# Performance work log

Hardware: AMD Instinct MI355X
Metric: run time of the kernel (lower is better)

## Reference

```python
import jax, jax.numpy as jnp
import numpy as np

CHUNK = 64   # hyperparams['chunk_size']
HEADS = 16   # hyperparams['n_heads']


def _chunk_mask(T, cs):
    # Faithful reproduction of the original (buggy) chunked mask:
    # for chunk pair with q-chunk start i and k-chunk start j, masking is applied
    # only when i >= j, with triu(diagonal = j - i + 1). Algebraically this masks
    # position (q, k) iff q_block_start >= k_block_start and
    #   (k - q) - 2*(k_block_start - q_block_start) >= 1.
    idx = jnp.arange(T)
    blk = (idx // cs) * cs  # chunk start of each position
    qb = blk[:, None]
    kb = blk[None, :]
    masked = (qb >= kb) & ((idx[None, :] - idx[:, None] - 2 * (kb - qb)) >= 1)
    return masked  # [T, T], True = set score to -inf


def setup_inputs() -> dict:
    key = jax.random.key(0)
    ks = jax.random.split(key, 6)
    B, T, C = 2, 2048, 1024
    w = 0.02  # init scale so softmax is not saturated
    return {
        "x": jax.random.normal(ks[0], (B, T, C), jnp.float32),
        "Wq": jax.random.normal(ks[1], (C, C), jnp.float32) * w,
        "bq": jnp.zeros((C,), jnp.float32),
        "Wk": jax.random.normal(ks[2], (C, C), jnp.float32) * w,
        "bk": jnp.zeros((C,), jnp.float32),
        "Wv": jax.random.normal(ks[3], (C, C), jnp.float32) * w,
        "bv": jnp.zeros((C,), jnp.float32),
        "Wo": jax.random.normal(ks[4], (C, C), jnp.float32) * w,
        "bo": jnp.zeros((C,), jnp.float32),
        "attn_scale": jnp.full((1,), 1.0 / np.sqrt(C // HEADS), jnp.float32),
    }


def reference(x, Wq, bq, Wk, bk, Wv, bv, Wo, bo, attn_scale):
    B, T, C = x.shape
    H = HEADS
    D = C // H
    # torch nn.Linear: y = x @ W.T + b
    q = (x @ Wq.T + bq).reshape(B, T, H, D)
    k = (x @ Wk.T + bk).reshape(B, T, H, D)
    v = (x @ Wv.T + bv).reshape(B, T, H, D)
    scores = jnp.einsum("bqhd,bkhd->bhqk", q, k) * attn_scale[0]
    mask = _chunk_mask(T, CHUNK)  # [T, T]
    scores = jnp.where(mask[None, None], -jnp.inf, scores)
    attn = jax.nn.softmax(scores, axis=-1)  # [B, H, T, T]
    out = jnp.einsum("bhqk,bkhd->bqhd", attn, v).reshape(B, T, C)
    return out @ Wo.T + bo
```

## Files before the change

### kernel.cpp

```cpp
#include <hip/hip_runtime.h>


typedef __attribute__((ext_vector_type(8))) short bf16x8;
typedef __attribute__((ext_vector_type(4))) float f32x4;
typedef __attribute__((ext_vector_type(4))) float float4v;
typedef __attribute__((ext_vector_type(4))) unsigned short u16x4;

__device__ __forceinline__ unsigned short f2bf(float x){
  union { float f; unsigned int u; } c; c.f = x;
  unsigned int r = c.u + 0x7FFFu + ((c.u >> 16) & 1u);
  return (unsigned short)(r >> 16);
}
__device__ __forceinline__ float bf2f(unsigned short h){
  union { unsigned int u; float f; } c; c.u = ((unsigned int)h) << 16;
  return c.f;
}
__device__ __forceinline__ f32x4 zero4(){ f32x4 v; v[0]=0.f; v[1]=0.f; v[2]=0.f; v[3]=0.f; return v; }
__device__ __forceinline__ unsigned int cvtpk(float a, float b){
  unsigned int r;
  asm("v_cvt_pk_bf16_f32 %0, %1, %2" : "=v"(r) : "v"(a), "v"(b));
  return r;
}
__device__ __forceinline__ float exp2x(float x){
  float r;
  asm("v_exp_f32 %0, %1" : "=v"(r) : "v"(x));
  return r;
}

#define GLDS16(g, l) __builtin_amdgcn_global_load_lds( \
  (const __attribute__((address_space(1))) void*)(g), \
  (__attribute__((address_space(3))) void*)(l), 16, 0, 0)

__global__ __launch_bounds__(256) void k_prep(
    const float* __restrict__ x,
    const float* __restrict__ Wq, const float* __restrict__ Wk,
    const float* __restrict__ Wv, const float* __restrict__ Wo,
    const float* __restrict__ bq, const float* __restrict__ bk, const float* __restrict__ bv,
    unsigned short* __restrict__ xh, unsigned short* __restrict__ wh,
    float* __restrict__ bias_cat){
  const int NX = 1048576;
  const int NTOT = 2097152;
  int i = blockIdx.x * 256 + threadIdx.x;
  if (i < 3072){
    const float* bs[3] = {bq, bk, bv};
    bias_cat[i] = bs[i >> 10][i & 1023];
  }
  int stride = gridDim.x * 256;
  for (; i < NTOT; i += stride){
    float4v v;
    u16x4 h;
    if (i < NX){
      v = ((const float4v*)x)[i];
      #pragma unroll
      for (int j = 0; j < 4; ++j) h[j] = f2bf(v[j]);
      ((u16x4*)xh)[i] = h;
    } else {
      int jj = i - NX;
      const float* srcs[4] = {Wq, Wk, Wv, Wo};
      v = ((const float4v*)srcs[jj >> 18])[jj & 0x3FFFF];
      #pragma unroll
      for (int j = 0; j < 4; ++j) h[j] = f2bf(v[j]);
      ((u16x4*)wh)[jj] = h;
    }
  }
}

template<int BM, int BN, int MODE, int SPLITA>
__global__ __launch_bounds__(256) void k_gemm(
    const unsigned short* __restrict__ Ah, const unsigned short* __restrict__ Al,
    const unsigned short* __restrict__ Bh,
    const float* __restrict__ bias, const float* __restrict__ scale_p,
    unsigned short* __restrict__ oq, unsigned short* __restrict__ okk,
    unsigned short* __restrict__ ov, float* __restrict__ fo)
{
  constexpr int MF = (BN == 128) ? (BM/32) : (BM/64);
  constexpr int NF = 4;
  constexpr int AISS = BM/64;
  constexpr int BISS = BN/64;
  constexpr int NA = SPLITA ? 2 : 1;
  __shared__ unsigned short As[NA][BM*32];
  __shared__ unsigned short Bs[BN*32];

  const int tid  = threadIdx.x;
  const int wid  = tid >> 6;
  const int lane = tid & 63;
  const int l15  = lane & 15;
  const int kg   = lane >> 4;
  const int m0 = blockIdx.y * BM;
  const int n0 = blockIdx.x * BN;
  const int wrb = (BN == 128) ? (wid >> 1) * (BM/2) : wid * (BM/4);
  const int wcb = (BN == 128) ? (wid & 1) * 64 : 0;
  const float qs = (MODE == 0) ? scale_p[0] * 1.4426950408889634f : 0.f;

  f32x4 acc[MF][NF];
  #pragma unroll
  for (int a = 0; a < MF; ++a)
    #pragma unroll
    for (int b = 0; b < NF; ++b) acc[a][b] = zero4();

  for (int k0 = 0; k0 < 1024; k0 += 32){
    #pragma unroll
    for (int p = 0; p < NA; ++p){
      const unsigned short* Asrc = p ? Al : Ah;
      #pragma unroll
      for (int iss = 0; iss < AISS; ++iss){
        int L = iss*2048 + tid*8;
        int row = L >> 5;
        int ck = ((L >> 3) & 3) ^ ((row >> 1) & 3);
        GLDS16(Asrc + (size_t)(m0 + row)*1024 + k0 + ck*8,
               (char*)(&As[p][0]) + iss*4096 + wid*1024);
      }
    }
    #pragma unroll
    for (int iss = 0; iss < BISS; ++iss){
      int L = iss*2048 + tid*8;
      int row = L >> 5;
      int ck = ((L >> 3) & 3) ^ ((row >> 1) & 3);
      GLDS16(Bh + (size_t)(n0 + row)*1024 + k0 + ck*8,
             (char*)(&Bs[0]) + iss*4096 + wid*1024);
    }
    __syncthreads();

    bf16x8 af[MF][NA];
    #pragma unroll
    for (int mf = 0; mf < MF; ++mf){
      int r = wrb + mf*16 + l15;
      int ckpos = kg ^ ((r >> 1) & 3);
      #pragma unroll
      for (int p = 0; p < NA; ++p)
        af[mf][p] = *(const bf16x8*)((const char*)(&As[p][0]) + r*64 + ckpos*16);
    }
    #pragma unroll
    for (int nf = 0; nf < NF; ++nf){
      int r = wcb + nf*16 + l15;
      int ckpos = kg ^ ((r >> 1) & 3);
      bf16x8 bhv = *(const bf16x8*)((const char*)(&Bs[0]) + r*64 + ckpos*16);
      #pragma unroll
      for (int mf = 0; mf < MF; ++mf){
        acc[mf][nf] = __builtin_amdgcn_mfma_f32_16x16x32_bf16(af[mf][0], bhv, acc[mf][nf], 0,0,0);
        if (SPLITA)
          acc[mf][nf] = __builtin_amdgcn_mfma_f32_16x16x32_bf16(af[mf][1], bhv, acc[mf][nf], 0,0,0);
      }
    }
    __syncthreads();
  }

  #pragma unroll
  for (int mf = 0; mf < MF; ++mf){
    #pragma unroll
    for (int nf = 0; nf < NF; ++nf){
      int colg = n0 + wcb + nf*16 + l15;
      float bb = bias[colg];
      #pragma unroll
      for (int j = 0; j < 4; ++j){
        int r = m0 + wrb + mf*16 + kg*4 + j;
        float val = acc[mf][nf][j] + bb;
        if (MODE == 1){
          fo[(size_t)r*1024 + colg] = val;
        } else {
          int bi = r >> 11, tt = r & 2047;
          int mat = colg >> 10, jj = colg & 1023;
          int h = jj >> 6, d = jj & 63;
          size_t bh_ = (size_t)(bi*16 + h);
          if (mat == 0)      oq [(bh_*2048 + tt)*64 + d] = f2bf(val * qs);
          else if (mat == 1) okk[(bh_*2048 + tt)*64 + d] = f2bf(val);
          else               ov [(bh_*64 + d)*2048 + tt] = f2bf(val);
        }
      }
    }
  }
}

__global__ __launch_bounds__(256) void k_attn(
    const unsigned short* __restrict__ Qg, const unsigned short* __restrict__ Kg,
    const unsigned short* __restrict__ Vtg,
    unsigned short* __restrict__ Ohi, unsigned short* __restrict__ Olo)
{
  __shared__ unsigned short Qs[64*64];
  __shared__ unsigned short Ks[2][64*64];
  __shared__ unsigned short Vts[2][64*64];

  const int tid  = threadIdx.x;
  const int wid  = tid >> 6;
  const int lane = tid & 63;
  const int l15  = lane & 15;
  const int kg   = lane >> 4;
  const int qi = blockIdx.x >> 5;
  const int bh = blockIdx.x & 31;
  const size_t base = (size_t)bh * (2048*64);

  const int r0 = tid >> 3;
  const int ck = ((tid & 7) ^ (r0 & 7)) * 8;
  const unsigned short* qp = Qg  + base + (size_t)(qi*64 + r0)*64 + ck;
  const unsigned short* kp = Kg  + base + (size_t)(qi*64 + r0)*64 + ck;
  const unsigned short* vp = Vtg + base + (size_t)r0*2048 + qi*64 + ck;

  GLDS16(qp,         (char*)Qs  + wid*1024);
  GLDS16(qp + 2048,  (char*)Qs  + wid*1024 + 4096);
  GLDS16(kp,         (char*)Ks  + wid*1024);
  GLDS16(kp + 2048,  (char*)Ks  + wid*1024 + 4096);
  GLDS16(vp,         (char*)Vts + wid*1024);
  GLDS16(vp + 65536, (char*)Vts + wid*1024 + 4096);
  kp += 4096;  vp += 64;
  __syncthreads();

  const int c0 = (kg ^ (l15 & 7)) << 4;
  const int c1 = c0 ^ 64;
  const char* qbase = (const char*)Qs + wid*2048 + l15*128;
  char* pwb = (char*)Qs + wid*2048 + l15*128;
  const int pws = (kg*8) ^ ((l15 & 7) << 4);

  const bf16x8 qf0 = *(const bf16x8*)(qbase + c0);
  const bf16x8 qf1 = *(const bf16x8*)(qbase + c1);

  f32x4 Ot[4];
  #pragma unroll
  for (int d = 0; d < 4; ++d) Ot[d] = zero4();
  float m = -1e30f, l = 0.f;
  const int qloc = wid*16 + l15;

  for (int kb = qi; kb < 32; ++kb){
    const int buf = (kb - qi) & 1;
    const char* ksb = (const char*)Ks  + buf*8192 + l15*128;
    const char* vsb = (const char*)Vts + buf*8192 + l15*128;
    if (kb + 1 < 32){
      char* dK = (char*)Ks  + (buf^1)*8192 + wid*1024;
      char* dV = (char*)Vts + (buf^1)*8192 + wid*1024;
      GLDS16(kp,         dK);
      GLDS16(kp + 2048,  dK + 4096);
      GLDS16(vp,         dV);
      GLDS16(vp + 65536, dV + 4096);
      kp += 4096;  vp += 64;
    }
    f32x4 ST[4];
    #pragma unroll
    for (int nf = 0; nf < 4; ++nf) ST[nf] = zero4();
    __builtin_amdgcn_s_setprio(1);
    #pragma unroll
    for (int nf = 0; nf < 4; ++nf){
      bf16x8 ak = *(const bf16x8*)(ksb + nf*2048 + c0);
      ST[nf] = __builtin_amdgcn_mfma_f32_16x16x32_bf16(ak, qf0, ST[nf], 0,0,0);
    }
    #pragma unroll
    for (int nf = 0; nf < 4; ++nf){
      bf16x8 ak = *(const bf16x8*)(ksb + nf*2048 + c1);
      ST[nf] = __builtin_amdgcn_mfma_f32_16x16x32_bf16(ak, qf1, ST[nf], 0,0,0);
    }
    __builtin_amdgcn_s_setprio(0);
    if (kb == qi){
      #pragma unroll
      for (int nf = 0; nf < 4; ++nf)
        #pragma unroll
        for (int j = 0; j < 4; ++j)
          if (nf*16 + kg*4 + j > qloc) ST[nf][j] = -1e30f;
    }
    float mx0 = fmaxf(fmaxf(ST[0][0], ST[0][1]), fmaxf(ST[0][2], ST[0][3]));
    float mx1 = fmaxf(fmaxf(ST[1][0], ST[1][1]), fmaxf(ST[1][2], ST[1][3]));
    float mx2 = fmaxf(fmaxf(ST[2][0], ST[2][1]), fmaxf(ST[2][2], ST[2][3]));
    float mx3 = fmaxf(fmaxf(ST[3][0], ST[3][1]), fmaxf(ST[3][2], ST[3][3]));
    float pmax = fmaxf(fmaxf(mx0, mx1), fmaxf(mx2, mx3));
    pmax = fmaxf(pmax, __shfl_xor(pmax, 16, 64));
    pmax = fmaxf(pmax, __shfl_xor(pmax, 32, 64));
    if (!__all(pmax <= m + 8.0f)){
      float mn = fmaxf(m, pmax);
      float fj = exp2x(m - mn);
      m = mn;
      l *= fj;
      #pragma unroll
      for (int df = 0; df < 4; ++df)
        #pragma unroll
        for (int j = 0; j < 4; ++j) Ot[df][j] *= fj;
    }
    float rsn[4];
    unsigned int pk[4][2];
    #pragma unroll
    for (int nf = 0; nf < 4; ++nf){
      float p0 = exp2x(ST[nf][0] - m), p1 = exp2x(ST[nf][1] - m);
      float p2 = exp2x(ST[nf][2] - m), p3 = exp2x(ST[nf][3] - m);
      rsn[nf] = (p0 + p1) + (p2 + p3);
      pk[nf][0] = cvtpk(p0, p1);
      pk[nf][1] = cvtpk(p2, p3);
    }
    float rs = (rsn[0] + rsn[1]) + (rsn[2] + rsn[3]);
    rs += __shfl_xor(rs, 16, 64);
    rs += __shfl_xor(rs, 32, 64);
    l += rs;
    #pragma unroll
    for (int nf = 0; nf < 4; ++nf)
      *(uint2*)(pwb + (pws ^ (nf*32))) = make_uint2(pk[nf][0], pk[nf][1]);
    {
      bf16x8 pa0 = *(const bf16x8*)(qbase + c0);
      bf16x8 pa1 = *(const bf16x8*)(qbase + c1);
      __builtin_amdgcn_s_setprio(1);
      #pragma unroll
      for (int df = 0; df < 4; ++df){
        bf16x8 vb = *(const bf16x8*)(vsb + df*2048 + c0);
        Ot[df] = __builtin_amdgcn_mfma_f32_16x16x32_bf16(vb, pa0, Ot[df], 0,0,0);
      }
      #pragma unroll
      for (int df = 0; df < 4; ++df){
        bf16x8 vb = *(const bf16x8*)(vsb + df*2048 + c1);
        Ot[df] = __builtin_amdgcn_mfma_f32_16x16x32_bf16(vb, pa1, Ot[df], 0,0,0);
      }
      __builtin_amdgcn_s_setprio(0);
    }
    __syncthreads();
  }

  const int bi = bh >> 4, h = bh & 15;
  const float rinv = 1.0f / l;
  const size_t row = (size_t)(bi*2048 + qi*64 + qloc);
  #pragma unroll
  for (int df = 0; df < 4; ++df){
    int colb = h*64 + df*16 + kg*4;
    u16x4 hv, lv;
    #pragma unroll
    for (int j = 0; j < 4; ++j){
      float v = Ot[df][j] * rinv;
      unsigned short hvv = f2bf(v);
      hv[j] = hvv;
      lv[j] = f2bf(v - bf2f(hvv));
    }
    *(u16x4*)(Ohi + row*1024 + colb) = hv;
    *(u16x4*)(Olo + row*1024 + colb) = lv;
  }
}

extern "C" void kernel_launch(void* const* d_in, const int* in_sizes, int n_in,
                              void* d_out, int out_size, void* d_ws, size_t ws_size,
                              hipStream_t stream){
  const float* x  = (const float*)d_in[0];
  const float* Wq = (const float*)d_in[1];
  const float* bq = (const float*)d_in[2];
  const float* Wk = (const float*)d_in[3];
  const float* bk = (const float*)d_in[4];
  const float* Wv = (const float*)d_in[5];
  const float* bv = (const float*)d_in[6];
  const float* Wo = (const float*)d_in[7];
  const float* bo = (const float*)d_in[8];
  const float* scale = (const float*)d_in[9];
  float* out = (float*)d_out;

  char* ws = (char*)d_ws;
  const size_t MB = 1024*1024;
  unsigned short* xh  = (unsigned short*)(ws + 0*MB);
  unsigned short* wh  = (unsigned short*)(ws + 16*MB);
  unsigned short* Qb  = (unsigned short*)(ws + 32*MB);
  unsigned short* Kb  = (unsigned short*)(ws + 40*MB);
  unsigned short* Vtb = (unsigned short*)(ws + 48*MB);
  unsigned short* Ohi = (unsigned short*)(ws + 56*MB);
  unsigned short* Olo = (unsigned short*)(ws + 64*MB);
  float* bias_cat     = (float*)(ws + 72*MB);

  hipLaunchKernelGGL(k_prep, dim3(2048), dim3(256), 0, stream,
                     x, Wq, Wk, Wv, Wo, bq, bk, bv, xh, wh, bias_cat);
  hipLaunchKernelGGL((k_gemm<128,128,0,0>), dim3(24,32), dim3(256), 0, stream,
                     xh, (const unsigned short*)nullptr, wh, bias_cat, scale,
                     Qb, Kb, Vtb, (float*)nullptr);
  hipLaunchKernelGGL(k_attn, dim3(1024), dim3(256), 0, stream, Qb, Kb, Vtb, Ohi, Olo);
  hipLaunchKernelGGL((k_gemm<64,64,1,1>), dim3(16,64), dim3(256), 0, stream,
                     Ohi, Olo, wh + 3u*1048576u, bo, (const float*)nullptr,
                     (unsigned short*)nullptr, (unsigned short*)nullptr,
                     (unsigned short*)nullptr, out);
}
```

Measured before the change: 205.9 us.

## Pair attention tiles per block and software-pipeline QK with triple-buffered K/V

Each attention block now handles two query tiles, pr and 31-pr, so the causal (upper-triangle) work is balanced across blocks, and the grid is halved. Inside the loop, QK^T for the next key tile is issued before the softmax and PV of the current tile. K and V use triple-buffered LDS with explicit vmcnt waits instead of __syncthreads, so loads and MFMA work overlap better. The cost is more LDS, more live registers (STn), and half as many blocks, which may leave some CUs idle.

```diff
diff --git a/kernel.cpp b/kernel.cpp
--- a/kernel.cpp
+++ b/kernel.cpp
@@ -25,6 +25,13 @@
   float r;
   asm("v_exp_f32 %0, %1" : "=v"(r) : "v"(x));
   return r;
+}
+__device__ __forceinline__ void wait_barrier(int n){
+  if (n == 4)      asm volatile("s_waitcnt vmcnt(4)" ::: "memory");
+  else if (n == 2) asm volatile("s_waitcnt vmcnt(2)" ::: "memory");
+  else             asm volatile("s_waitcnt vmcnt(0)" ::: "memory");
+  __builtin_amdgcn_s_barrier();
+  __builtin_amdgcn_sched_barrier(0);
 }
 
 #define GLDS16(g, l) __builtin_amdgcn_global_load_lds( \
@@ -176,153 +183,204 @@
     const unsigned short* __restrict__ Vtg,
     unsigned short* __restrict__ Ohi, unsigned short* __restrict__ Olo)
 {
-  __shared__ unsigned short Qs[64*64];
-  __shared__ unsigned short Ks[2][64*64];
-  __shared__ unsigned short Vts[2][64*64];
+  __shared__ unsigned short Qs[4096];
+  __shared__ unsigned short Ks[3][4096];
+  __shared__ unsigned short Vts[3][4096];
 
   const int tid  = threadIdx.x;
   const int wid  = tid >> 6;
   const int lane = tid & 63;
   const int l15  = lane & 15;
   const int kg   = lane >> 4;
-  const int qi = blockIdx.x >> 5;
+  const int pr = blockIdx.x >> 5;
   const int bh = blockIdx.x & 31;
   const size_t base = (size_t)bh * (2048*64);
 
   const int r0 = tid >> 3;
   const int ck = ((tid & 7) ^ (r0 & 7)) * 8;
-  const unsigned short* qp = Qg  + base + (size_t)(qi*64 + r0)*64 + ck;
-  const unsigned short* kp = Kg  + base + (size_t)(qi*64 + r0)*64 + ck;
-  const unsigned short* vp = Vtg + base + (size_t)r0*2048 + qi*64 + ck;
-
-  GLDS16(qp,         (char*)Qs  + wid*1024);
-  GLDS16(qp + 2048,  (char*)Qs  + wid*1024 + 4096);
-  GLDS16(kp,         (char*)Ks  + wid*1024);
-  GLDS16(kp + 2048,  (char*)Ks  + wid*1024 + 4096);
-  GLDS16(vp,         (char*)Vts + wid*1024);
-  GLDS16(vp + 65536, (char*)Vts + wid*1024 + 4096);
-  kp += 4096;  vp += 64;
-  __syncthreads();
-
   const int c0 = (kg ^ (l15 & 7)) << 4;
   const int c1 = c0 ^ 64;
   const char* qbase = (const char*)Qs + wid*2048 + l15*128;
   char* pwb = (char*)Qs + wid*2048 + l15*128;
   const int pws = (kg*8) ^ ((l15 & 7) << 4);
-
-  const bf16x8 qf0 = *(const bf16x8*)(qbase + c0);
-  const bf16x8 qf1 = *(const bf16x8*)(qbase + c1);
-
-  f32x4 Ot[4];
-  #pragma unroll
-  for (int d = 0; d < 4; ++d) Ot[d] = zero4();
-  float m = -1e30f, l = 0.f;
   const int qloc = wid*16 + l15;
-
-  for (int kb = qi; kb < 32; ++kb){
-    const int buf = (kb - qi) & 1;
-    const char* ksb = (const char*)Ks  + buf*8192 + l15*128;
-    const char* vsb = (const char*)Vts + buf*8192 + l15*128;
-    if (kb + 1 < 32){
-      char* dK = (char*)Ks  + (buf^1)*8192 + wid*1024;
-      char* dV = (char*)Vts + (buf^1)*8192 + wid*1024;
-      GLDS16(kp,         dK);
-      GLDS16(kp + 2048,  dK + 4096);
-      GLDS16(vp,         dV);
-      GLDS16(vp + 65536, dV + 4096);
-      kp += 4096;  vp += 64;
-    }
+  const int bi = bh >> 4, h = bh & 15;
+
+  #pragma unroll 1
+  for (int half = 0; half < 2; ++half){
+    const int t0 = half ? (31 - pr) : pr;
+    const unsigned short* qp  = Qg  + base + (size_t)(t0*64 + r0)*64 + ck;
+    const unsigned short* kp0 = Kg  + base + (size_t)(t0*64 + r0)*64 + ck;
+    const unsigned short* vp0 = Vtg + base + (size_t)r0*2048 + t0*64 + ck;
+    GLDS16(qp,          (char*)Qs + wid*1024);
+    GLDS16(qp + 2048,   (char*)Qs + wid*1024 + 4096);
+    GLDS16(kp0,         (char*)(&Ks[0][0]) + wid*1024);
+    GLDS16(kp0 + 2048,  (char*)(&Ks[0][0]) + wid*1024 + 4096);
+    GLDS16(vp0,         (char*)(&Vts[0][0]) + wid*1024);
+    GLDS16(vp0 + 65536, (char*)(&Vts[0][0]) + wid*1024 + 4096);
+    int nA = 0;
+    if (t0 + 1 <= 31){
+      GLDS16(kp0 + 4096, (char*)(&Ks[1][0]) + wid*1024);
+      GLDS16(kp0 + 6144, (char*)(&Ks[1][0]) + wid*1024 + 4096);
+      nA = 2;
+    }
+    wait_barrier(nA);
+
+    const bf16x8 qf0 = *(const bf16x8*)(qbase + c0);
+    const bf16x8 qf1 = *(const bf16x8*)(qbase + c1);
+
     f32x4 ST[4];
     #pragma unroll
     for (int nf = 0; nf < 4; ++nf) ST[nf] = zero4();
-    __builtin_amdgcn_s_setprio(1);
-    #pragma unroll
-    for (int nf = 0; nf < 4; ++nf){
-      bf16x8 ak = *(const bf16x8*)(ksb + nf*2048 + c0);
-      ST[nf] = __builtin_amdgcn_mfma_f32_16x16x32_bf16(ak, qf0, ST[nf], 0,0,0);
-    }
-    #pragma unroll
-    for (int nf = 0; nf < 4; ++nf){
-      bf16x8 ak = *(const bf16x8*)(ksb + nf*2048 + c1);
-      ST[nf] = __builtin_amdgcn_mfma_f32_16x16x32_bf16(ak, qf1, ST[nf], 0,0,0);
-    }
-    __builtin_amdgcn_s_setprio(0);
-    if (kb == qi){
+    {
+      const char* ksb = (const char*)(&Ks[0][0]) + l15*128;
+      __builtin_amdgcn_s_setprio(1);
+      #pragma unroll
+      for (int nf = 0; nf < 4; ++nf){
+        bf16x8 ak = *(const bf16x8*)(ksb + nf*2048 + c0);
+        ST[nf] = __builtin_amdgcn_mfma_f32_16x16x32_bf16(ak, qf0, ST[nf], 0,0,0);
+      }
+      #pragma unroll
+      for (int nf = 0; nf < 4; ++nf){
+        bf16x8 ak = *(const bf16x8*)(ksb + nf*2048 + c1);
+        ST[nf] = __builtin_amdgcn_mfma_f32_16x16x32_bf16(ak, qf1, ST[nf], 0,0,0);
+      }
+      __builtin_amdgcn_s_setprio(0);
+    }
+    #pragma unroll
+    for (int nf = 0; nf < 4; ++nf)
+      #pragma unroll
+      for (int j = 0; j < 4; ++j)
+        if (nf*16 + kg*4 + j > qloc) ST[nf][j] = -1e30f;
+
+    int nB = 0;
+    if (t0 + 1 <= 31){
+      GLDS16(vp0 + 64,         (char*)(&Vts[1][0]) + wid*1024);
+      GLDS16(vp0 + 64 + 65536, (char*)(&Vts[1][0]) + wid*1024 + 4096);
+      nB += 2;
+    }
+    if (t0 + 2 <= 31){
+      GLDS16(kp0 + 8192,  (char*)(&Ks[2][0]) + wid*1024);
+      GLDS16(kp0 + 10240, (char*)(&Ks[2][0]) + wid*1024 + 4096);
+      nB += 2;
+    }
+    wait_barrier(nB);
+
+    f32x4 Ot[4];
+    #pragma unroll
+    for (int d = 0; d < 4; ++d) Ot[d] = zero4();
+    float m = -1e30f, l = 0.f;
+    const unsigned short* kp = kp0 + 12288;
+    const unsigned short* vp = vp0 + 128;
+    int s0 = 0, s1 = 1, s2 = 2;
+
+    for (int kb = t0; kb < 32; ++kb){
+      int nIss = 0;
+      if (kb + 3 <= 31){
+        char* dK = (char*)(&Ks[s0][0]) + wid*1024;
+        GLDS16(kp, dK);
+        GLDS16(kp + 2048, dK + 4096);
+        kp += 4096; nIss += 2;
+      }
+      if (kb + 2 <= 31){
+        char* dV = (char*)(&Vts[s2][0]) + wid*1024;
+        GLDS16(vp, dV);
+        GLDS16(vp + 65536, dV + 4096);
+        vp += 64; nIss += 2;
+      }
+      f32x4 STn[4];
+      if (kb < 31){
+        const char* ksb = (const char*)(&Ks[s1][0]) + l15*128;
+        #pragma unroll
+        for (int nf = 0; nf < 4; ++nf) STn[nf] = zero4();
+        __builtin_amdgcn_s_setprio(1);
+        #pragma unroll
+        for (int nf = 0; nf < 4; ++nf){
+          bf16x8 ak = *(const bf16x8*)(ksb + nf*2048 + c0);
+          STn[nf] = __builtin_amdgcn_mfma_f32_16x16x32_bf16(ak, qf0, STn[nf], 0,0,0);
+        }
+        #pragma unroll
+        for (int nf = 0; nf < 4; ++nf){
+          bf16x8 ak = *(const bf16x8*)(ksb + nf*2048 + c1);
+          STn[nf] = __builtin_amdgcn_mfma_f32_16x16x32_bf16(ak, qf1, STn[nf], 0,0,0);
+        }
+        __builtin_amdgcn_s_setprio(0);
+      }
+      float mx0 = fmaxf(fmaxf(ST[0][0], ST[0][1]), fmaxf(ST[0][2], ST[0][3]));
+      float mx1 = fmaxf(fmaxf(ST[1][0], ST[1][1]), fmaxf(ST[1][2], ST[1][3]));
+      float mx2 = fmaxf(fmaxf(ST[2][0], ST[2][1]), fmaxf(ST[2][2], ST[2][3]));
+      float mx3 = fmaxf(fmaxf(ST[3][0], ST[3][1]), fmaxf(ST[3][2], ST[3][3]));
+      float pmax = fmaxf(fmaxf(mx0, mx1), fmaxf(mx2, mx3));
+      pmax = fmaxf(pmax, __shfl_xor(pmax, 16, 64));
+      pmax = fmaxf(pmax, __shfl_xor(pmax, 32, 64));
+      if (!__all(pmax <= m + 8.0f)){
+        float mn = fmaxf(m, pmax);
+        float fj = exp2x(m - mn);
+        m = mn;
+        l *= fj;
+        #pragma unroll
+        for (int df = 0; df < 4; ++df)
+          #pragma unroll
+          for (int j = 0; j < 4; ++j) Ot[df][j] *= fj;
+      }
+      float rsn[4];
+      unsigned int pk[4][2];
+      #pragma unroll
+      for (int nf = 0; nf < 4; ++nf){
+        float p0 = exp2x(ST[nf][0] - m), p1 = exp2x(ST[nf][1] - m);
+        float p2 = exp2x(ST[nf][2] - m), p3 = exp2x(ST[nf][3] - m);
+        rsn[nf] = (p0 + p1) + (p2 + p3);
+        pk[nf][0] = cvtpk(p0, p1);
+        pk[nf][1] = cvtpk(p2, p3);
+      }
+      float rs = (rsn[0] + rsn[1]) + (rsn[2] + rsn[3]);
+      rs += __shfl_xor(rs, 16, 64);
+      rs += __shfl_xor(rs, 32, 64);
+      l += rs;
       #pragma unroll
       for (int nf = 0; nf < 4; ++nf)
-        #pragma unroll
-        for (int j = 0; j < 4; ++j)
-          if (nf*16 + kg*4 + j > qloc) ST[nf][j] = -1e30f;
-    }
-    float mx0 = fmaxf(fmaxf(ST[0][0], ST[0][1]), fmaxf(ST[0][2], ST[0][3]));
-    float mx1 = fmaxf(fmaxf(ST[1][0], ST[1][1]), fmaxf(ST[1][2], ST[1][3]));
-    float mx2 = fmaxf(fmaxf(ST[2][0], ST[2][1]), fmaxf(ST[2][2], ST[2][3]));
-    float mx3 = fmaxf(fmaxf(ST[3][0], ST[3][1]), fmaxf(ST[3][2], ST[3][3]));
-    float pmax = fmaxf(fmaxf(mx0, mx1), fmaxf(mx2, mx3));
-    pmax = fmaxf(pmax, __shfl_xor(pmax, 16, 64));
-    pmax = fmaxf(pmax, __shfl_xor(pmax, 32, 64));
-    if (!__all(pmax <= m + 8.0f)){
-      float mn = fmaxf(m, pmax);
-      float fj = exp2x(m - mn);
-      m = mn;
-      l *= fj;
-      #pragma unroll
-      for (int df = 0; df < 4; ++df)
-        #pragma unroll
-        for (int j = 0; j < 4; ++j) Ot[df][j] *= fj;
-    }
-    float rsn[4];
-    unsigned int pk[4][2];
-    #pragma unroll
-    for (int nf = 0; nf < 4; ++nf){
-      float p0 = exp2x(ST[nf][0] - m), p1 = exp2x(ST[nf][1] - m);
-      float p2 = exp2x(ST[nf][2] - m), p3 = exp2x(ST[nf][3] - m);
-      rsn[nf] = (p0 + p1) + (p2 + p3);
-      pk[nf][0] = cvtpk(p0, p1);
-      pk[nf][1] = cvtpk(p2, p3);
-    }
-    float rs = (rsn[0] + rsn[1]) + (rsn[2] + rsn[3]);
-    rs += __shfl_xor(rs, 16, 64);
-    rs += __shfl_xor(rs, 32, 64);
-    l += rs;
-    #pragma unroll
-    for (int nf = 0; nf < 4; ++nf)
-      *(uint2*)(pwb + (pws ^ (nf*32))) = make_uint2(pk[nf][0], pk[nf][1]);
-    {
-      bf16x8 pa0 = *(const bf16x8*)(qbase + c0);
-      bf16x8 pa1 = *(const bf16x8*)(qbase + c1);
-      __builtin_amdgcn_s_setprio(1);
-      #pragma unroll
-      for (int df = 0; df < 4; ++df){
-        bf16x8 vb = *(const bf16x8*)(vsb + df*2048 + c0);
-        Ot[df] = __builtin_amdgcn_mfma_f32_16x16x32_bf16(vb, pa0, Ot[df], 0,0,0);
-      }
-      #pragma unroll
-      for (int df = 0; df < 4; ++df){
-        bf16x8 vb = *(const bf16x8*)(vsb + df*2048 + c1);
-        Ot[df] = __builtin_amdgcn_mfma_f32_16x16x32_bf16(vb, pa1, Ot[df], 0,0,0);
-      }
-      __builtin_amdgcn_s_setprio(0);
-    }
-    __syncthreads();
-  }
-
-  const int bi = bh >> 4, h = bh & 15;
-  const float rinv = 1.0f / l;
-  const size_t row = (size_t)(bi*2048 + qi*64 + qloc);
-  #pragma unroll
-  for (int df = 0; df < 4; ++df){
-    int colb = h*64 + df*16 + kg*4;
-    u16x4 hv, lv;
-    #pragma unroll
-    for (int j = 0; j < 4; ++j){
-      float v = Ot[df][j] * rinv;
-      unsigned short hvv = f2bf(v);
-      hv[j] = hvv;
-      lv[j] = f2bf(v - bf2f(hvv));
-    }
-    *(u16x4*)(Ohi + row*1024 + colb) = hv;
-    *(u16x4*)(Olo + row*1024 + colb) = lv;
+        *(uint2*)(pwb + (pws ^ (nf*32))) = make_uint2(pk[nf][0], pk[nf][1]);
+      {
+        bf16x8 pa0 = *(const bf16x8*)(qbase + c0);
+        bf16x8 pa1 = *(const bf16x8*)(qbase + c1);
+        const char* vsb = (const char*)(&Vts[s0][0]) + l15*128;
+        __builtin_amdgcn_s_setprio(1);
+        #pragma unroll
+        for (int df = 0; df < 4; ++df){
+          bf16x8 vb = *(const bf16x8*)(vsb + df*2048 + c0);
+          Ot[df] = __builtin_amdgcn_mfma_f32_16x16x32_bf16(vb, pa0, Ot[df], 0,0,0);
+        }
+        #pragma unroll
+        for (int df = 0; df < 4; ++df){
+          bf16x8 vb = *(const bf16x8*)(vsb + df*2048 + c1);
+          Ot[df] = __builtin_amdgcn_mfma_f32_16x16x32_bf16(vb, pa1, Ot[df], 0,0,0);
+        }
+        __builtin_amdgcn_s_setprio(0);
+      }
+      if (kb < 31){
+        #pragma unroll
+        for (int nf = 0; nf < 4; ++nf) ST[nf] = STn[nf];
+      }
+      int tmp = s0; s0 = s1; s1 = s2; s2 = tmp;
+      wait_barrier(nIss);
+    }
+
+    const float rinv = 1.0f / l;
+    const size_t row = (size_t)(bi*2048 + t0*64 + qloc);
+    #pragma unroll
+    for (int df = 0; df < 4; ++df){
+      int colb = h*64 + df*16 + kg*4;
+      u16x4 hv, lv;
+      #pragma unroll
+      for (int j = 0; j < 4; ++j){
+        float v = Ot[df][j] * rinv;
+        unsigned short hvv = f2bf(v);
+        hv[j] = hvv;
+        lv[j] = f2bf(v - bf2f(hvv));
+      }
+      *(u16x4*)(Ohi + row*1024 + colb) = hv;
+      *(u16x4*)(Olo + row*1024 + colb) = lv;
+    }
   }
 }
 
@@ -357,7 +415,7 @@
   hipLaunchKernelGGL((k_gemm<128,128,0,0>), dim3(24,32), dim3(256), 0, stream,
                      xh, (const unsigned short*)nullptr, wh, bias_cat, scale,
                      Qb, Kb, Vtb, (float*)nullptr);
-  hipLaunchKernelGGL(k_attn, dim3(1024), dim3(256), 0, stream, Qb, Kb, Vtb, Ohi, Olo);
+  hipLaunchKernelGGL(k_attn, dim3(512), dim3(256), 0, stream, Qb, Kb, Vtb, Ohi, Olo);
   hipLaunchKernelGGL((k_gemm<64,64,1,1>), dim3(16,64), dim3(256), 0, stream,
                      Ohi, Olo, wh + 3u*1048576u, bo, (const float*)nullptr,
                      (unsigned short*)nullptr, (unsigned short*)nullptr,
```

Result: slower. 210.7 us (+2.3%).

## Process two query chunks per attention block with balanced tile pairing

Applied to the files above, without the earlier changes.

Each attention workgroup now handles two adjacent 64-row query chunks, so one K/V tile load from global memory and LDS serves both chunks. Query tiles are assigned in pairs (p and 23-p style mapping) to even out the triangular work across blocks, and the grid is halved to 512 blocks. The output projection GEMM also switches to a 128x64 tile with half the grid. Costs are more registers per thread (two accumulator sets), twice the LDS for Q, and fewer blocks to fill the GPU.

```diff
diff --git a/kernel.cpp b/kernel.cpp
--- a/kernel.cpp
+++ b/kernel.cpp
@@ -171,32 +171,87 @@
   }
 }
 
+#define SOFTMAX_STEP(ST_, m_, l_, O_, pw_) do { \
+  float _x0 = fmaxf(fmaxf(ST_[0][0],ST_[0][1]), fmaxf(ST_[0][2],ST_[0][3])); \
+  float _x1 = fmaxf(fmaxf(ST_[1][0],ST_[1][1]), fmaxf(ST_[1][2],ST_[1][3])); \
+  float _x2 = fmaxf(fmaxf(ST_[2][0],ST_[2][1]), fmaxf(ST_[2][2],ST_[2][3])); \
+  float _x3 = fmaxf(fmaxf(ST_[3][0],ST_[3][1]), fmaxf(ST_[3][2],ST_[3][3])); \
+  float _pm = fmaxf(fmaxf(_x0,_x1), fmaxf(_x2,_x3)); \
+  _pm = fmaxf(_pm, __shfl_xor(_pm, 16, 64)); \
+  _pm = fmaxf(_pm, __shfl_xor(_pm, 32, 64)); \
+  if (!__all(_pm <= m_ + 8.0f)){ \
+    float _mn = fmaxf(m_, _pm); \
+    float _fj = exp2x(m_ - _mn); \
+    m_ = _mn; l_ *= _fj; \
+    _Pragma("unroll") \
+    for (int _d = 0; _d < 4; ++_d) \
+      _Pragma("unroll") \
+      for (int _j = 0; _j < 4; ++_j) O_[_d][_j] *= _fj; \
+  } \
+  unsigned int _pk[4][2]; \
+  float _rt = 0.f; \
+  _Pragma("unroll") \
+  for (int _n = 0; _n < 4; ++_n){ \
+    float _p0 = exp2x(ST_[_n][0] - m_), _p1 = exp2x(ST_[_n][1] - m_); \
+    float _p2 = exp2x(ST_[_n][2] - m_), _p3 = exp2x(ST_[_n][3] - m_); \
+    _rt += (_p0 + _p1) + (_p2 + _p3); \
+    _pk[_n][0] = cvtpk(_p0, _p1); \
+    _pk[_n][1] = cvtpk(_p2, _p3); \
+  } \
+  _rt += __shfl_xor(_rt, 16, 64); \
+  _rt += __shfl_xor(_rt, 32, 64); \
+  l_ += _rt; \
+  _Pragma("unroll") \
+  for (int _n = 0; _n < 4; ++_n) \
+    *(uint2*)(pw_ + (pws ^ (_n*32))) = make_uint2(_pk[_n][0], _pk[_n][1]); \
+} while(0)
+
+#define QK_STEP(ST_, qlo_, qhi_) do { \
+  _Pragma("unroll") \
+  for (int _n = 0; _n < 4; ++_n) ST_[_n] = zero4(); \
+  __builtin_amdgcn_s_setprio(1); \
+  _Pragma("unroll") \
+  for (int _n = 0; _n < 4; ++_n){ \
+    bf16x8 _ak = *(const bf16x8*)(ksb + _n*2048 + c0); \
+    ST_[_n] = __builtin_amdgcn_mfma_f32_16x16x32_bf16(_ak, qlo_, ST_[_n], 0,0,0); \
+  } \
+  _Pragma("unroll") \
+  for (int _n = 0; _n < 4; ++_n){ \
+    bf16x8 _ak = *(const bf16x8*)(ksb + _n*2048 + c1); \
+    ST_[_n] = __builtin_amdgcn_mfma_f32_16x16x32_bf16(_ak, qhi_, ST_[_n], 0,0,0); \
+  } \
+  __builtin_amdgcn_s_setprio(0); \
+} while(0)
+
 __global__ __launch_bounds__(256) void k_attn(
     const unsigned short* __restrict__ Qg, const unsigned short* __restrict__ Kg,
     const unsigned short* __restrict__ Vtg,
     unsigned short* __restrict__ Ohi, unsigned short* __restrict__ Olo)
 {
-  __shared__ unsigned short Qs[64*64];
-  __shared__ unsigned short Ks[2][64*64];
-  __shared__ unsigned short Vts[2][64*64];
+  __shared__ unsigned short Qs[8192];
+  __shared__ unsigned short Ks[2][4096];
+  __shared__ unsigned short Vts[2][4096];
 
   const int tid  = threadIdx.x;
   const int wid  = tid >> 6;
   const int lane = tid & 63;
   const int l15  = lane & 15;
   const int kg   = lane >> 4;
-  const int qi = blockIdx.x >> 5;
+  const int p  = blockIdx.x >> 5;
+  const int qt = (p < 8) ? p : 23 - p;
   const int bh = blockIdx.x & 31;
   const size_t base = (size_t)bh * (2048*64);
+  const int qc0 = 2*qt, qc1 = 2*qt + 1;
 
   const int r0 = tid >> 3;
   const int ck = ((tid & 7) ^ (r0 & 7)) * 8;
-  const unsigned short* qp = Qg  + base + (size_t)(qi*64 + r0)*64 + ck;
-  const unsigned short* kp = Kg  + base + (size_t)(qi*64 + r0)*64 + ck;
-  const unsigned short* vp = Vtg + base + (size_t)r0*2048 + qi*64 + ck;
-
-  GLDS16(qp,         (char*)Qs  + wid*1024);
-  GLDS16(qp + 2048,  (char*)Qs  + wid*1024 + 4096);
+  const unsigned short* qp = Qg  + base + (size_t)(qc0*64 + r0)*64 + ck;
+  const unsigned short* kp = Kg  + base + (size_t)(qc0*64 + r0)*64 + ck;
+  const unsigned short* vp = Vtg + base + (size_t)r0*2048 + qc0*64 + ck;
+  GLDS16(qp,         (char*)Qs + wid*1024);
+  GLDS16(qp + 2048,  (char*)Qs + wid*1024 + 4096);
+  GLDS16(qp + 4096,  (char*)Qs + wid*1024 + 8192);
+  GLDS16(qp + 6144,  (char*)Qs + wid*1024 + 12288);
   GLDS16(kp,         (char*)Ks  + wid*1024);
   GLDS16(kp + 2048,  (char*)Ks  + wid*1024 + 4096);
   GLDS16(vp,         (char*)Vts + wid*1024);
@@ -206,23 +261,28 @@
 
   const int c0 = (kg ^ (l15 & 7)) << 4;
   const int c1 = c0 ^ 64;
-  const char* qbase = (const char*)Qs + wid*2048 + l15*128;
-  char* pwb = (char*)Qs + wid*2048 + l15*128;
+  const char* qb0 = (const char*)Qs + wid*2048 + l15*128;
+  const char* qb1 = qb0 + 8192;
+  char* pw0 = (char*)Qs + wid*2048 + l15*128;
+  char* pw1 = pw0 + 8192;
   const int pws = (kg*8) ^ ((l15 & 7) << 4);
-
-  const bf16x8 qf0 = *(const bf16x8*)(qbase + c0);
-  const bf16x8 qf1 = *(const bf16x8*)(qbase + c1);
-
-  f32x4 Ot[4];
+  const int qloc = wid*16 + l15;
+
+  const bf16x8 qA0 = *(const bf16x8*)(qb0 + c0);
+  const bf16x8 qA1 = *(const bf16x8*)(qb0 + c1);
+  const bf16x8 qB0 = *(const bf16x8*)(qb1 + c0);
+  const bf16x8 qB1 = *(const bf16x8*)(qb1 + c1);
+
+  f32x4 O0[4], O1[4];
   #pragma unroll
-  for (int d = 0; d < 4; ++d) Ot[d] = zero4();
-  float m = -1e30f, l = 0.f;
-  const int qloc = wid*16 + l15;
-
-  for (int kb = qi; kb < 32; ++kb){
-    const int buf = (kb - qi) & 1;
+  for (int d = 0; d < 4; ++d){ O0[d] = zero4(); O1[d] = zero4(); }
+  float m0 = -1e30f, l0 = 0.f, m1 = -1e30f, l1 = 0.f;
+
+  for (int kb = qc0; kb < 32; ++kb){
+    const int buf = (kb - qc0) & 1;
     const char* ksb = (const char*)Ks  + buf*8192 + l15*128;
     const char* vsb = (const char*)Vts + buf*8192 + l15*128;
+    const bool act1 = (kb >= qc1);
     if (kb + 1 < 32){
       char* dK = (char*)Ks  + (buf^1)*8192 + wid*1024;
       char* dV = (char*)Vts + (buf^1)*8192 + wid*1024;
@@ -232,97 +292,88 @@
       GLDS16(vp + 65536, dV + 4096);
       kp += 4096;  vp += 64;
     }
-    f32x4 ST[4];
-    #pragma unroll
-    for (int nf = 0; nf < 4; ++nf) ST[nf] = zero4();
-    __builtin_amdgcn_s_setprio(1);
-    #pragma unroll
-    for (int nf = 0; nf < 4; ++nf){
-      bf16x8 ak = *(const bf16x8*)(ksb + nf*2048 + c0);
-      ST[nf] = __builtin_amdgcn_mfma_f32_16x16x32_bf16(ak, qf0, ST[nf], 0,0,0);
-    }
-    #pragma unroll
-    for (int nf = 0; nf < 4; ++nf){
-      bf16x8 ak = *(const bf16x8*)(ksb + nf*2048 + c1);
-      ST[nf] = __builtin_amdgcn_mfma_f32_16x16x32_bf16(ak, qf1, ST[nf], 0,0,0);
-    }
-    __builtin_amdgcn_s_setprio(0);
-    if (kb == qi){
-      #pragma unroll
-      for (int nf = 0; nf < 4; ++nf)
-        #pragma unroll
-        for (int j = 0; j < 4; ++j)
-          if (nf*16 + kg*4 + j > qloc) ST[nf][j] = -1e30f;
-    }
-    float mx0 = fmaxf(fmaxf(ST[0][0], ST[0][1]), fmaxf(ST[0][2], ST[0][3]));
-    float mx1 = fmaxf(fmaxf(ST[1][0], ST[1][1]), fmaxf(ST[1][2], ST[1][3]));
-    float mx2 = fmaxf(fmaxf(ST[2][0], ST[2][1]), fmaxf(ST[2][2], ST[2][3]));
-    float mx3 = fmaxf(fmaxf(ST[3][0], ST[3][1]), fmaxf(ST[3][2], ST[3][3]));
-    float pmax = fmaxf(fmaxf(mx0, mx1), fmaxf(mx2, mx3));
-    pmax = fmaxf(pmax, __shfl_xor(pmax, 16, 64));
-    pmax = fmaxf(pmax, __shfl_xor(pmax, 32, 64));
-    if (!__all(pmax <= m + 8.0f)){
-      float mn = fmaxf(m, pmax);
-      float fj = exp2x(m - mn);
-      m = mn;
-      l *= fj;
-      #pragma unroll
-      for (int df = 0; df < 4; ++df)
-        #pragma unroll
-        for (int j = 0; j < 4; ++j) Ot[df][j] *= fj;
-    }
-    float rsn[4];
-    unsigned int pk[4][2];
-    #pragma unroll
-    for (int nf = 0; nf < 4; ++nf){
-      float p0 = exp2x(ST[nf][0] - m), p1 = exp2x(ST[nf][1] - m);
-      float p2 = exp2x(ST[nf][2] - m), p3 = exp2x(ST[nf][3] - m);
-      rsn[nf] = (p0 + p1) + (p2 + p3);
-      pk[nf][0] = cvtpk(p0, p1);
-      pk[nf][1] = cvtpk(p2, p3);
-    }
-    float rs = (rsn[0] + rsn[1]) + (rsn[2] + rsn[3]);
-    rs += __shfl_xor(rs, 16, 64);
-    rs += __shfl_xor(rs, 32, 64);
-    l += rs;
-    #pragma unroll
-    for (int nf = 0; nf < 4; ++nf)
-      *(uint2*)(pwb + (pws ^ (nf*32))) = make_uint2(pk[nf][0], pk[nf][1]);
     {
-      bf16x8 pa0 = *(const bf16x8*)(qbase + c0);
-      bf16x8 pa1 = *(const bf16x8*)(qbase + c1);
-      __builtin_amdgcn_s_setprio(1);
-      #pragma unroll
-      for (int df = 0; df < 4; ++df){
-        bf16x8 vb = *(const bf16x8*)(vsb + df*2048 + c0);
-        Ot[df] = __builtin_amdgcn_mfma_f32_16x16x32_bf16(vb, pa0, Ot[df], 0,0,0);
-      }
-      #pragma unroll
-      for (int df = 0; df < 4; ++df){
-        bf16x8 vb = *(const bf16x8*)(vsb + df*2048 + c1);
-        Ot[df] = __builtin_amdgcn_mfma_f32_16x16x32_bf16(vb, pa1, Ot[df], 0,0,0);
-      }
-      __builtin_amdgcn_s_setprio(0);
+      f32x4 ST[4];
+      QK_STEP(ST, qA0, qA1);
+      if (kb == qc0){
+        #pragma unroll
+        for (int nf = 0; nf < 4; ++nf)
+          #pragma unroll
+          for (int j = 0; j < 4; ++j)
+            if (nf*16 + kg*4 + j > qloc) ST[nf][j] = -1e30f;
+      }
+      SOFTMAX_STEP(ST, m0, l0, O0, pw0);
+    }
+    if (act1){
+      f32x4 ST[4];
+      QK_STEP(ST, qB0, qB1);
+      if (kb == qc1){
+        #pragma unroll
+        for (int nf = 0; nf < 4; ++nf)
+          #pragma unroll
+          for (int j = 0; j < 4; ++j)
+            if (nf*16 + kg*4 + j > qloc) ST[nf][j] = -1e30f;
+      }
+      SOFTMAX_STEP(ST, m1, l1, O1, pw1);
+    }
+    {
+      bf16x8 pa00 = *(const bf16x8*)(qb0 + c0);
+      bf16x8 pa01 = *(const bf16x8*)(qb0 + c1);
+      if (act1){
+        bf16x8 pa10 = *(const bf16x8*)(qb1 + c0);
+        bf16x8 pa11 = *(const bf16x8*)(qb1 + c1);
+        __builtin_amdgcn_s_setprio(1);
+        #pragma unroll
+        for (int df = 0; df < 4; ++df){
+          bf16x8 vb = *(const bf16x8*)(vsb + df*2048 + c0);
+          O0[df] = __builtin_amdgcn_mfma_f32_16x16x32_bf16(vb, pa00, O0[df], 0,0,0);
+          O1[df] = __builtin_amdgcn_mfma_f32_16x16x32_bf16(vb, pa10, O1[df], 0,0,0);
+        }
+        #pragma unroll
+        for (int df = 0; df < 4; ++df){
+          bf16x8 vb = *(const bf16x8*)(vsb + df*2048 + c1);
+          O0[df] = __builtin_amdgcn_mfma_f32_16x16x32_bf16(vb, pa01, O0[df], 0,0,0);
+          O1[df] = __builtin_amdgcn_mfma_f32_16x16x32_bf16(vb, pa11, O1[df], 0,0,0);
+        }
+        __builtin_amdgcn_s_setprio(0);
+      } else {
+        __builtin_amdgcn_s_setprio(1);
+        #pragma unroll
+        for (int df = 0; df < 4; ++df){
+          bf16x8 vb = *(const bf16x8*)(vsb + df*2048 + c0);
+          O0[df] = __builtin_amdgcn_mfma_f32_16x16x32_bf16(vb, pa00, O0[df], 0,0,0);
+        }
+        #pragma unroll
+        for (int df = 0; df < 4; ++df){
+          bf16x8 vb = *(const bf16x8*)(vsb + df*2048 + c1);
+          O0[df] = __builtin_amdgcn_mfma_f32_16x16x32_bf16(vb, pa01, O0[df], 0,0,0);
+        }
+        __builtin_amdgcn_s_setprio(0);
+      }
     }
     __syncthreads();
   }
 
   const int bi = bh >> 4, h = bh & 15;
-  const float rinv = 1.0f / l;
-  const size_t row = (size_t)(bi*2048 + qi*64 + qloc);
   #pragma unroll
-  for (int df = 0; df < 4; ++df){
-    int colb = h*64 + df*16 + kg*4;
-    u16x4 hv, lv;
-    #pragma unroll
-    for (int j = 0; j < 4; ++j){
-      float v = Ot[df][j] * rinv;
-      unsigned short hvv = f2bf(v);
-      hv[j] = hvv;
-      lv[j] = f2bf(v - bf2f(hvv));
-    }
-    *(u16x4*)(Ohi + row*1024 + colb) = hv;
-    *(u16x4*)(Olo + row*1024 + colb) = lv;
+  for (int set = 0; set < 2; ++set){
+    const float rinv = 1.0f / (set ? l1 : l0);
+    const f32x4* O = set ? O1 : O0;
+    const size_t row = (size_t)(bi*2048 + (qc0 + set)*64 + qloc);
+    #pragma unroll
+    for (int df = 0; df < 4; ++df){
+      int colb = h*64 + df*16 + kg*4;
+      u16x4 hv, lv;
+      #pragma unroll
+      for (int j = 0; j < 4; ++j){
+        float v = O[df][j] * rinv;
+        unsigned short hvv = f2bf(v);
+        hv[j] = hvv;
+        lv[j] = f2bf(v - bf2f(hvv));
+      }
+      *(u16x4*)(Ohi + row*1024 + colb) = hv;
+      *(u16x4*)(Olo + row*1024 + colb) = lv;
+    }
   }
 }
 
@@ -357,8 +408,8 @@
   hipLaunchKernelGGL((k_gemm<128,128,0,0>), dim3(24,32), dim3(256), 0, stream,
                      xh, (const unsigned short*)nullptr, wh, bias_cat, scale,
                      Qb, Kb, Vtb, (float*)nullptr);
-  hipLaunchKernelGGL(k_attn, dim3(1024), dim3(256), 0, stream, Qb, Kb, Vtb, Ohi, Olo);
-  hipLaunchKernelGGL((k_gemm<64,64,1,1>), dim3(16,64), dim3(256), 0, stream,
+  hipLaunchKernelGGL(k_attn, dim3(512), dim3(256), 0, stream, Qb, Kb, Vtb, Ohi, Olo);
+  hipLaunchKernelGGL((k_gemm<128,64,1,1>), dim3(16,32), dim3(256), 0, stream,
                      Ohi, Olo, wh + 3u*1048576u, bo, (const float*)nullptr,
                      (unsigned short*)nullptr, (unsigned short*)nullptr,
                      (unsigned short*)nullptr, out);
```

Result: slower. 219.9 us (+6.8%).
